# Kernel optimization log

Measured on AMD Instinct MI355X. Metric: run time of the kernel, lower is better.

## Reference

```python
import jax, jax.numpy as jnp
import numpy as np

LN_EPS = 1e-5

def layer_norm(h, gamma, beta):
    mu = jnp.mean(h, axis=-1, keepdims=True)
    var = jnp.mean(jnp.square(h - mu), axis=-1, keepdims=True)
    return (h - mu) * jax.lax.rsqrt(var + LN_EPS) * gamma + beta

def gcn_conv(x, src, dst, W, b, n_nodes):
    # PyG GCNConv: h = X W; out = D^-1/2 (A + I) D^-1/2 h + b
    h = x @ W
    deg = jax.ops.segment_sum(jnp.ones_like(src, dtype=h.dtype), dst, num_segments=n_nodes)
    dinv = jax.lax.rsqrt(jnp.maximum(deg, 1.0))  # deg >= 1 due to self-loops
    norm = dinv[src] * dinv[dst]                  # [E]
    msg = h[src] * norm[:, None]                  # [E, d]
    return jax.ops.segment_sum(msg, dst, num_segments=n_nodes) + b

def setup_inputs() -> dict:
    key = jax.random.key(0)
    ks = jax.random.split(key, 8)
    N, E, Cin, Ch, Cout = 10000, 160000, 256, 512, 256
    x = jax.random.normal(ks[0], (N, Cin), dtype=jnp.float32)
    edge_index = jax.random.randint(ks[1], (2, E), 0, N, dtype=jnp.int64)
    W1 = jax.random.normal(ks[2], (Cin, Ch), dtype=jnp.float32) * (1.0 / np.sqrt(Cin))
    b1 = jnp.zeros((Ch,), dtype=jnp.float32)
    gamma1 = jnp.ones((Ch,), dtype=jnp.float32)
    beta1 = jnp.zeros((Ch,), dtype=jnp.float32)
    W2 = jax.random.normal(ks[3], (Ch, Cout), dtype=jnp.float32) * (1.0 / np.sqrt(Ch))
    b2 = jnp.zeros((Cout,), dtype=jnp.float32)
    gamma2 = jnp.ones((Cout,), dtype=jnp.float32)
    beta2 = jnp.zeros((Cout,), dtype=jnp.float32)
    return {"x": x, "edge_index": edge_index, "W1": W1, "b1": b1,
            "gamma1": gamma1, "beta1": beta1, "W2": W2, "b2": b2,
            "gamma2": gamma2, "beta2": beta2}

def reference(x, edge_index, W1, b1, gamma1, beta1, W2, b2, gamma2, beta2):
    n = x.shape[0]
    loops = jnp.arange(n, dtype=edge_index.dtype)
    src = jnp.concatenate([edge_index[0], loops])
    dst = jnp.concatenate([edge_index[1], loops])
    h = gcn_conv(x, src, dst, W1, b1, n)
    h = jax.nn.relu(layer_norm(h, gamma1, beta1))  # dropout = identity (eval mode)
    g = gcn_conv(h, src, dst, W2, b2, n)
    g = jax.nn.relu(layer_norm(g, gamma2, beta2))
    return g
```

## Files before the change

### kernel.cpp

```cpp
#include <hip/hip_runtime.h>
#include <hip/hip_bf16.h>


typedef __attribute__((ext_vector_type(8))) short bf16x8;
typedef __attribute__((ext_vector_type(4))) float f32x4;
typedef __attribute__((ext_vector_type(4))) unsigned short us4;

__device__ __forceinline__ unsigned short f2bf(float f) {
  unsigned int x = __float_as_uint(f);
  return (unsigned short)((x + 0x7FFFu + ((x >> 16) & 1u)) >> 16);
}

__device__ __forceinline__ void wave_reduce2(float& s, float& ss) {
#pragma unroll
  for (int off = 32; off > 0; off >>= 1) {
    s  += __shfl_down(s, off, 64);
    ss += __shfl_down(ss, off, 64);
  }
}


__global__ __launch_bounds__(256) void deg_kernel(const int* __restrict__ dst, int E,
                                                  int* __restrict__ deg) {
  int e = blockIdx.x * 256 + threadIdx.x;
  if (e < E) atomicAdd(&deg[dst[e]], 1);
}

__global__ __launch_bounds__(256) void dinv_kernel(const int* __restrict__ deg, int N,
                                                   float* __restrict__ dinv) {
  int i = blockIdx.x * 256 + threadIdx.x;
  if (i < N) dinv[i] = rsqrtf((float)(deg[i] + 1));
}

__global__ __launch_bounds__(1024) void scan_kernel(const int* __restrict__ deg, int N,
                                                    int* __restrict__ offsets) {
  __shared__ int wsum[16];
  __shared__ int chunk_base;
  int tid = threadIdx.x;
  int lane = tid & 63, wid = tid >> 6;
  if (tid == 0) chunk_base = 0;
  __syncthreads();
  for (int c = 0; c < N; c += 1024) {
    int i = c + tid;
    int v = (i < N) ? deg[i] : 0;
    int s = v;
#pragma unroll
    for (int off = 1; off < 64; off <<= 1) {
      int t = __shfl_up(s, off, 64);
      if (lane >= off) s += t;
    }
    if (lane == 63) wsum[wid] = s;
    __syncthreads();
    if (wid == 0 && lane < 16) {
      int ws = wsum[lane];
      int t = ws;
#pragma unroll
      for (int off = 1; off < 16; off <<= 1) {
        int u = __shfl_up(t, off, 64);
        if (lane >= off) t += u;
      }
      wsum[lane] = t - ws;
    }
    __syncthreads();
    if (i < N) offsets[i] = chunk_base + wsum[wid] + s - v;
    __syncthreads();
    if (tid == 1023) chunk_base += wsum[15] + s;
  }
  __syncthreads();
  if (tid == 0) offsets[N] = chunk_base;
}

__global__ __launch_bounds__(256) void fill_kernel(const int* __restrict__ src,
                                                   const int* __restrict__ dst, int E,
                                                   const int* __restrict__ offsets,
                                                   int* __restrict__ cursor,
                                                   const float* __restrict__ dinv,
                                                   int* __restrict__ csr_src,
                                                   float* __restrict__ csr_norm) {
  int e = blockIdx.x * 256 + threadIdx.x;
  if (e >= E) return;
  int s = src[e], d = dst[e];
  int p = offsets[d] + atomicAdd(&cursor[d], 1);
  csr_src[p]  = s;
  csr_norm[p] = dinv[s] * dinv[d];
}


template <typename OutT>
__global__ __launch_bounds__(256) void agg_kernel(const float* __restrict__ H,
                                                  const int* __restrict__ csr_src,
                                                  const float* __restrict__ csr_norm,
                                                  const int* __restrict__ offsets,
                                                  const float* __restrict__ dinv,
                                                  const float* __restrict__ bias,
                                                  OutT* __restrict__ out) {
  __shared__ f32x4 sh[256];
  int node = blockIdx.x;
  int tid = threadIdx.x, w = tid >> 6, c4 = tid & 63;
  int p0 = offsets[node], p1 = offsets[node + 1];
  f32x4 acc = {0.f, 0.f, 0.f, 0.f};
  for (int p = p0 + w; p < p1; p += 4) {
    int s   = csr_src[p];
    float wt = csr_norm[p];
    f32x4 h = *(const f32x4*)&H[(size_t)s * 256 + c4 * 4];
    acc += h * wt;
  }
  sh[tid] = acc;
  __syncthreads();
  if (tid < 64) {
    f32x4 a = sh[tid] + sh[64 + tid] + sh[128 + tid] + sh[192 + tid];
    float dn = dinv[node];
    f32x4 self = *(const f32x4*)&H[(size_t)node * 256 + tid * 4];
    a += self * (dn * dn);
    if (bias) a += *(const f32x4*)&bias[tid * 4];
    if constexpr (sizeof(OutT) == 4) {
      *(f32x4*)&out[(size_t)node * 256 + tid * 4] = a;
    } else {
      us4 o;
      o.x = f2bf(a.x); o.y = f2bf(a.y); o.z = f2bf(a.z); o.w = f2bf(a.w);
      *(us4*)&out[(size_t)node * 256 + tid * 4] = o;
    }
  }
}

__global__ __launch_bounds__(256) void transpose_bf16(const float* __restrict__ W,
                                                      unsigned short* __restrict__ Wt,
                                                      int K, int N) {
  __shared__ unsigned short t[32][33];
  int n0 = blockIdx.x * 32, k0 = blockIdx.y * 32;
  int tx = threadIdx.x & 31, ty = threadIdx.x >> 5;
#pragma unroll
  for (int i = 0; i < 32; i += 8)
    t[ty + i][tx] = f2bf(W[(size_t)(k0 + ty + i) * N + n0 + tx]);
  __syncthreads();
#pragma unroll
  for (int i = 0; i < 32; i += 8)
    Wt[(size_t)(n0 + ty + i) * K + k0 + tx] = t[tx][ty + i];
}


__global__ __launch_bounds__(256) void mfma_gemm_kernel(
    const unsigned short* __restrict__ A, const unsigned short* __restrict__ Bt,
    const float* __restrict__ bias, float* __restrict__ C, int M, int K, int N) {
  __shared__ unsigned short As[128 * 32];
  __shared__ unsigned short Bs[128 * 32];
  int tid = threadIdx.x;
  int lane = tid & 63, wid = tid >> 6;
  int bm = blockIdx.x * 128, bn = blockIdx.y * 128;
  int wm = (wid >> 1) * 64, wn = (wid & 1) * 64;
  int srow = tid >> 2;
  int schunk = tid & 3;
  int frow = lane & 15, fk = lane >> 4;
  f32x4 acc[4][4] = {};

  for (int k0 = 0; k0 < K; k0 += 32) {
#pragma unroll
    for (int r = 0; r < 2; ++r) {
      int row = r * 64 + srow;
      int scA = schunk ^ ((row >> 1) & 3);
      int ga = bm + row; ga = ga < M ? ga : M - 1;
      int gb = bn + row; gb = gb < N ? gb : N - 1;
      const unsigned short* gA = A + (size_t)ga * K + k0 + scA * 8;
      const unsigned short* gB = Bt + (size_t)gb * K + k0 + scA * 8;
      __builtin_amdgcn_global_load_lds(
          (const __attribute__((address_space(1))) unsigned int*)(const void*)gA,
          (__attribute__((address_space(3))) unsigned int*)(void*)(As + (r * 64 + wid * 16) * 32),
          16, 0, 0);
      __builtin_amdgcn_global_load_lds(
          (const __attribute__((address_space(1))) unsigned int*)(const void*)gB,
          (__attribute__((address_space(3))) unsigned int*)(void*)(Bs + (r * 64 + wid * 16) * 32),
          16, 0, 0);
    }
    __syncthreads();
    bf16x8 af[4], bf[4];
#pragma unroll
    for (int mi = 0; mi < 4; ++mi) {
      int row = wm + mi * 16 + frow;
      int sc = fk ^ ((row >> 1) & 3);
      af[mi] = *(const bf16x8*)(As + row * 32 + sc * 8);
    }
#pragma unroll
    for (int ni = 0; ni < 4; ++ni) {
      int row = wn + ni * 16 + frow;
      int sc = fk ^ ((row >> 1) & 3);
      bf[ni] = *(const bf16x8*)(Bs + row * 32 + sc * 8);
    }
#pragma unroll
    for (int mi = 0; mi < 4; ++mi)
#pragma unroll
      for (int ni = 0; ni < 4; ++ni)
        acc[mi][ni] = __builtin_amdgcn_mfma_f32_16x16x32_bf16(af[mi], bf[ni], acc[mi][ni], 0, 0, 0);
    __syncthreads();
  }

  int row0 = bm + wm + (lane >> 4) * 4;
  int col0 = bn + wn + (lane & 15);
#pragma unroll
  for (int mi = 0; mi < 4; ++mi) {
#pragma unroll
    for (int ni = 0; ni < 4; ++ni) {
      int col = col0 + ni * 16;
      float bv = bias ? bias[col] : 0.0f;
#pragma unroll
      for (int r = 0; r < 4; ++r) {
        int row = row0 + mi * 16 + r;
        if (row < M) C[(size_t)row * N + col] = acc[mi][ni][r] + bv;
      }
    }
  }
}


template <int C, typename OutT>
__global__ __launch_bounds__(256) void ln_relu_kernel(const float* __restrict__ in,
                                                      const float* __restrict__ gamma,
                                                      const float* __restrict__ beta,
                                                      OutT* __restrict__ out) {
  int row = blockIdx.x;
  const float* p = in + (size_t)row * C;
  int tid = threadIdx.x;
  float v0 = p[tid];
  float v1 = (C == 512) ? p[tid + 256] : 0.0f;
  float s = v0 + v1;
  float ss = v0 * v0 + v1 * v1;
  wave_reduce2(s, ss);
  __shared__ float sh[8];
  int wid = tid >> 6;
  if ((tid & 63) == 0) { sh[wid] = s; sh[4 + wid] = ss; }
  __syncthreads();
  s  = sh[0] + sh[1] + sh[2] + sh[3];
  ss = sh[4] + sh[5] + sh[6] + sh[7];
  float mu = s * (1.0f / C);
  float var = ss * (1.0f / C) - mu * mu;
  float r = rsqrtf(var + 1e-5f);
  float o0 = fmaxf((v0 - mu) * r * gamma[tid] + beta[tid], 0.0f);
  if constexpr (sizeof(OutT) == 4) out[(size_t)row * C + tid] = o0;
  else                             out[(size_t)row * C + tid] = f2bf(o0);
  if (C == 512) {
    float o1 = fmaxf((v1 - mu) * r * gamma[tid + 256] + beta[tid + 256], 0.0f);
    if constexpr (sizeof(OutT) == 4) out[(size_t)row * C + tid + 256] = o1;
    else                             out[(size_t)row * C + tid + 256] = f2bf(o1);
  }
}


extern "C" void kernel_launch(void* const* d_in, const int* in_sizes, int n_in,
                              void* d_out, int out_size, void* d_ws, size_t ws_size,
                              hipStream_t stream) {
  const float* x    = (const float*)d_in[0];
  const int*   ei   = (const int*)d_in[1];
  const float* W1   = (const float*)d_in[2];
  const float* b1   = (const float*)d_in[3];
  const float* ga1  = (const float*)d_in[4];
  const float* be1  = (const float*)d_in[5];
  const float* W2   = (const float*)d_in[6];
  const float* b2   = (const float*)d_in[7];
  const float* ga2  = (const float*)d_in[8];
  const float* be2  = (const float*)d_in[9];
  float* out = (float*)d_out;

  const int Ch   = in_sizes[3];
  const int Cout = in_sizes[7];
  const int Cin  = in_sizes[2] / Ch;
  const int N    = in_sizes[0] / Cin;
  const int E    = in_sizes[1] / 2;
  const int* srcp = ei;
  const int* dstp = ei + E;

  char* ws = (char*)d_ws;
  size_t off = 0;
  auto alloc = [&](size_t bytes) -> void* {
    off = (off + 255) & ~(size_t)255;
    void* p = ws + off;
    off += bytes;
    return p;
  };
  unsigned short* axb  = (unsigned short*)alloc((size_t)N * Cin * 2);
  float*          h1   = (float*)alloc((size_t)N * Ch * 4);
  unsigned short* h1b  = (unsigned short*)alloc((size_t)N * Ch * 2);
  float*          h2   = (float*)alloc((size_t)N * Cout * 4);
  unsigned short* W1t  = (unsigned short*)alloc((size_t)Cin * Ch * 2);
  unsigned short* W2t  = (unsigned short*)alloc((size_t)Ch * Cout * 2);
  int*   deg   = (int*)alloc((size_t)N * 4);
  int*   curs  = (int*)alloc((size_t)N * 4);
  int*   offs  = (int*)alloc((size_t)(N + 1) * 4);
  float* dinv  = (float*)alloc((size_t)N * 4);
  int*   csr_s = (int*)alloc((size_t)E * 4);
  float* csr_n = (float*)alloc((size_t)E * 4);

  hipMemsetAsync(deg, 0, (size_t)N * 4, stream);
  hipMemsetAsync(curs, 0, (size_t)N * 4, stream);

  int gE = (E + 255) / 256;
  int gN = (N + 255) / 256;
  deg_kernel<<<gE, 256, 0, stream>>>(dstp, E, deg);
  dinv_kernel<<<gN, 256, 0, stream>>>(deg, N, dinv);
  scan_kernel<<<1, 1024, 0, stream>>>(deg, N, offs);
  fill_kernel<<<gE, 256, 0, stream>>>(srcp, dstp, E, offs, curs, dinv, csr_s, csr_n);

  transpose_bf16<<<dim3(Ch / 32, Cin / 32), 256, 0, stream>>>(W1, W1t, Cin, Ch);
  transpose_bf16<<<dim3(Cout / 32, Ch / 32), 256, 0, stream>>>(W2, W2t, Ch, Cout);

  agg_kernel<unsigned short><<<N, 256, 0, stream>>>(x, csr_s, csr_n, offs, dinv, nullptr, axb);
  mfma_gemm_kernel<<<dim3((N + 127) / 128, Ch / 128), 256, 0, stream>>>(axb, W1t, b1, h1, N, Cin, Ch);
  ln_relu_kernel<512, unsigned short><<<N, 256, 0, stream>>>(h1, ga1, be1, h1b);

  mfma_gemm_kernel<<<dim3((N + 127) / 128, Cout / 128), 256, 0, stream>>>(h1b, W2t, nullptr, h2, N, Ch, Cout);
  agg_kernel<float><<<N, 256, 0, stream>>>(h2, csr_s, csr_n, offs, dinv, b2, h1);
  ln_relu_kernel<256, float><<<N, 256, 0, stream>>>(h1, ga2, be2, out);
}
```

Before: 222.0 us.

## Fuse preprocessing kernels, gather bf16 features, fuse final LayerNorm into aggregation

Merges the degree count, the x-to-bf16 cast and both weight transposes into one multi-role prep kernel, and folds dinv computation and cursor initialisation into the scan. Aggregation now gathers bf16 rows instead of fp32, which halves gather traffic. The second GEMM writes bf16 output, and the final LayerNorm+ReLU is fused into the second aggregation kernel. This removes several launches and intermediate round trips through memory, at the cost of extra bf16 rounding on the gathered features and one more workspace buffer.

Measured after the change: 208.4 us. 1.07x faster.

```diff
diff --git a/kernel.cpp b/kernel.cpp
--- a/kernel.cpp
+++ b/kernel.cpp
@@ -5,35 +5,68 @@
 typedef __attribute__((ext_vector_type(8))) short bf16x8;
 typedef __attribute__((ext_vector_type(4))) float f32x4;
 typedef __attribute__((ext_vector_type(4))) unsigned short us4;
+typedef __attribute__((ext_vector_type(8))) unsigned short us8;
 
 __device__ __forceinline__ unsigned short f2bf(float f) {
   unsigned int x = __float_as_uint(f);
   return (unsigned short)((x + 0x7FFFu + ((x >> 16) & 1u)) >> 16);
 }
-
-__device__ __forceinline__ void wave_reduce2(float& s, float& ss) {
-#pragma unroll
-  for (int off = 32; off > 0; off >>= 1) {
-    s  += __shfl_down(s, off, 64);
-    ss += __shfl_down(ss, off, 64);
-  }
-}
-
-
-__global__ __launch_bounds__(256) void deg_kernel(const int* __restrict__ dst, int E,
-                                                  int* __restrict__ deg) {
-  int e = blockIdx.x * 256 + threadIdx.x;
-  if (e < E) atomicAdd(&deg[dst[e]], 1);
-}
-
-__global__ __launch_bounds__(256) void dinv_kernel(const int* __restrict__ deg, int N,
-                                                   float* __restrict__ dinv) {
-  int i = blockIdx.x * 256 + threadIdx.x;
-  if (i < N) dinv[i] = rsqrtf((float)(deg[i] + 1));
+__device__ __forceinline__ float bf2f(unsigned short u) {
+  return __uint_as_float((unsigned int)u << 16);
+}
+
+
+__device__ __forceinline__ void transpose_tile(const float* __restrict__ W,
+                                               unsigned short* __restrict__ Wt,
+                                               int K, int N, int n0, int k0,
+                                               unsigned short (*t)[33], int tid) {
+  int tx = tid & 31, ty = tid >> 5;
+#pragma unroll
+  for (int i = 0; i < 32; i += 8)
+    t[ty + i][tx] = f2bf(W[(size_t)(k0 + ty + i) * N + n0 + tx]);
+  __syncthreads();
+#pragma unroll
+  for (int i = 0; i < 32; i += 8)
+    Wt[(size_t)(n0 + ty + i) * K + k0 + tx] = t[tx][ty + i];
+}
+
+__global__ __launch_bounds__(256) void prep_kernel(
+    const float* __restrict__ x, unsigned short* __restrict__ xb, long nelem,
+    const int* __restrict__ dst, int E, int* __restrict__ deg,
+    const float* __restrict__ W1, unsigned short* __restrict__ W1t,
+    const float* __restrict__ W2, unsigned short* __restrict__ W2t,
+    int Cin, int Ch, int Cout, int nbx, int nbe, int nbw1) {
+  __shared__ unsigned short t[32][33];
+  int bid = blockIdx.x;
+  int tid = threadIdx.x;
+  if (bid < nbx) {
+    long i = ((long)bid * 256 + tid) * 8;
+    if (i + 8 <= nelem) {
+      f32x4 a = *(const f32x4*)&x[i];
+      f32x4 b = *(const f32x4*)&x[i + 4];
+      us8 o;
+      o[0] = f2bf(a.x); o[1] = f2bf(a.y); o[2] = f2bf(a.z); o[3] = f2bf(a.w);
+      o[4] = f2bf(b.x); o[5] = f2bf(b.y); o[6] = f2bf(b.z); o[7] = f2bf(b.w);
+      *(us8*)&xb[i] = o;
+    }
+  } else if (bid < nbx + nbe) {
+    int e = (bid - nbx) * 256 + tid;
+    if (e < E) atomicAdd(&deg[dst[e]], 1);
+  } else if (bid < nbx + nbe + nbw1) {
+    int ti = bid - nbx - nbe;
+    int w1w = Ch >> 5;
+    transpose_tile(W1, W1t, Cin, Ch, (ti % w1w) * 32, (ti / w1w) * 32, t, tid);
+  } else {
+    int ti = bid - nbx - nbe - nbw1;
+    int w2w = Cout >> 5;
+    transpose_tile(W2, W2t, Ch, Cout, (ti % w2w) * 32, (ti / w2w) * 32, t, tid);
+  }
 }
 
 __global__ __launch_bounds__(1024) void scan_kernel(const int* __restrict__ deg, int N,
-                                                    int* __restrict__ offsets) {
+                                                    int* __restrict__ offsets,
+                                                    int* __restrict__ curs,
+                                                    float* __restrict__ dinv) {
   __shared__ int wsum[16];
   __shared__ int chunk_base;
   int tid = threadIdx.x;
@@ -43,6 +76,7 @@
   for (int c = 0; c < N; c += 1024) {
     int i = c + tid;
     int v = (i < N) ? deg[i] : 0;
+    if (i < N) dinv[i] = rsqrtf((float)(v + 1));
     int s = v;
 #pragma unroll
     for (int off = 1; off < 64; off <<= 1) {
@@ -62,7 +96,11 @@
       wsum[lane] = t - ws;
     }
     __syncthreads();
-    if (i < N) offsets[i] = chunk_base + wsum[wid] + s - v;
+    if (i < N) {
+      int o = chunk_base + wsum[wid] + s - v;
+      offsets[i] = o;
+      curs[i] = o;
+    }
     __syncthreads();
     if (tid == 1023) chunk_base += wsum[15] + s;
   }
@@ -72,27 +110,28 @@
 
 __global__ __launch_bounds__(256) void fill_kernel(const int* __restrict__ src,
                                                    const int* __restrict__ dst, int E,
-                                                   const int* __restrict__ offsets,
-                                                   int* __restrict__ cursor,
+                                                   int* __restrict__ curs,
                                                    const float* __restrict__ dinv,
                                                    int* __restrict__ csr_src,
                                                    float* __restrict__ csr_norm) {
   int e = blockIdx.x * 256 + threadIdx.x;
   if (e >= E) return;
   int s = src[e], d = dst[e];
-  int p = offsets[d] + atomicAdd(&cursor[d], 1);
+  int p = atomicAdd(&curs[d], 1);
   csr_src[p]  = s;
   csr_norm[p] = dinv[s] * dinv[d];
 }
 
 
-template <typename OutT>
-__global__ __launch_bounds__(256) void agg_kernel(const float* __restrict__ H,
+template <bool FUSE_LN, typename OutT>
+__global__ __launch_bounds__(256) void agg_kernel(const unsigned short* __restrict__ H,
                                                   const int* __restrict__ csr_src,
                                                   const float* __restrict__ csr_norm,
                                                   const int* __restrict__ offsets,
                                                   const float* __restrict__ dinv,
                                                   const float* __restrict__ bias,
+                                                  const float* __restrict__ gamma,
+                                                  const float* __restrict__ beta,
                                                   OutT* __restrict__ out) {
   __shared__ f32x4 sh[256];
   int node = blockIdx.x;
@@ -100,21 +139,45 @@
   int p0 = offsets[node], p1 = offsets[node + 1];
   f32x4 acc = {0.f, 0.f, 0.f, 0.f};
   for (int p = p0 + w; p < p1; p += 4) {
-    int s   = csr_src[p];
+    int s    = csr_src[p];
     float wt = csr_norm[p];
-    f32x4 h = *(const f32x4*)&H[(size_t)s * 256 + c4 * 4];
-    acc += h * wt;
+    us4 hv = *(const us4*)&H[(size_t)s * 256 + c4 * 4];
+    acc.x = fmaf(bf2f(hv.x), wt, acc.x);
+    acc.y = fmaf(bf2f(hv.y), wt, acc.y);
+    acc.z = fmaf(bf2f(hv.z), wt, acc.z);
+    acc.w = fmaf(bf2f(hv.w), wt, acc.w);
   }
   sh[tid] = acc;
   __syncthreads();
   if (tid < 64) {
     f32x4 a = sh[tid] + sh[64 + tid] + sh[128 + tid] + sh[192 + tid];
     float dn = dinv[node];
-    f32x4 self = *(const f32x4*)&H[(size_t)node * 256 + tid * 4];
-    a += self * (dn * dn);
+    float w2 = dn * dn;
+    us4 sv = *(const us4*)&H[(size_t)node * 256 + tid * 4];
+    a.x = fmaf(bf2f(sv.x), w2, a.x);
+    a.y = fmaf(bf2f(sv.y), w2, a.y);
+    a.z = fmaf(bf2f(sv.z), w2, a.z);
+    a.w = fmaf(bf2f(sv.w), w2, a.w);
     if (bias) a += *(const f32x4*)&bias[tid * 4];
-    if constexpr (sizeof(OutT) == 4) {
-      *(f32x4*)&out[(size_t)node * 256 + tid * 4] = a;
+    if constexpr (FUSE_LN) {
+      float s  = a.x + a.y + a.z + a.w;
+      float ss = a.x * a.x + a.y * a.y + a.z * a.z + a.w * a.w;
+#pragma unroll
+      for (int off = 32; off > 0; off >>= 1) {
+        s  += __shfl_xor(s, off, 64);
+        ss += __shfl_xor(ss, off, 64);
+      }
+      float mu = s * (1.0f / 256.0f);
+      float var = ss * (1.0f / 256.0f) - mu * mu;
+      float r = rsqrtf(var + 1e-5f);
+      f32x4 g  = *(const f32x4*)&gamma[tid * 4];
+      f32x4 be = *(const f32x4*)&beta[tid * 4];
+      f32x4 o;
+      o.x = fmaxf((a.x - mu) * r * g.x + be.x, 0.f);
+      o.y = fmaxf((a.y - mu) * r * g.y + be.y, 0.f);
+      o.z = fmaxf((a.z - mu) * r * g.z + be.z, 0.f);
+      o.w = fmaxf((a.w - mu) * r * g.w + be.w, 0.f);
+      *(f32x4*)&out[(size_t)node * 256 + tid * 4] = o;
     } else {
       us4 o;
       o.x = f2bf(a.x); o.y = f2bf(a.y); o.z = f2bf(a.z); o.w = f2bf(a.w);
@@ -123,25 +186,11 @@
   }
 }
 
-__global__ __launch_bounds__(256) void transpose_bf16(const float* __restrict__ W,
-                                                      unsigned short* __restrict__ Wt,
-                                                      int K, int N) {
-  __shared__ unsigned short t[32][33];
-  int n0 = blockIdx.x * 32, k0 = blockIdx.y * 32;
-  int tx = threadIdx.x & 31, ty = threadIdx.x >> 5;
-#pragma unroll
-  for (int i = 0; i < 32; i += 8)
-    t[ty + i][tx] = f2bf(W[(size_t)(k0 + ty + i) * N + n0 + tx]);
-  __syncthreads();
-#pragma unroll
-  for (int i = 0; i < 32; i += 8)
-    Wt[(size_t)(n0 + ty + i) * K + k0 + tx] = t[tx][ty + i];
-}
-
-
+
+template <typename OutT>
 __global__ __launch_bounds__(256) void mfma_gemm_kernel(
     const unsigned short* __restrict__ A, const unsigned short* __restrict__ Bt,
-    const float* __restrict__ bias, float* __restrict__ C, int M, int K, int N) {
+    const float* __restrict__ bias, OutT* __restrict__ C, int M, int K, int N) {
   __shared__ unsigned short As[128 * 32];
   __shared__ unsigned short Bs[128 * 32];
   int tid = threadIdx.x;
@@ -204,43 +253,44 @@
 #pragma unroll
       for (int r = 0; r < 4; ++r) {
         int row = row0 + mi * 16 + r;
-        if (row < M) C[(size_t)row * N + col] = acc[mi][ni][r] + bv;
+        if (row < M) {
+          float v = acc[mi][ni][r] + bv;
+          if constexpr (sizeof(OutT) == 4) C[(size_t)row * N + col] = v;
+          else                             C[(size_t)row * N + col] = f2bf(v);
+        }
       }
     }
   }
 }
 
 
-template <int C, typename OutT>
-__global__ __launch_bounds__(256) void ln_relu_kernel(const float* __restrict__ in,
-                                                      const float* __restrict__ gamma,
-                                                      const float* __restrict__ beta,
-                                                      OutT* __restrict__ out) {
+__global__ __launch_bounds__(256) void ln_relu512_kernel(const float* __restrict__ in,
+                                                         const float* __restrict__ gamma,
+                                                         const float* __restrict__ beta,
+                                                         unsigned short* __restrict__ out) {
   int row = blockIdx.x;
-  const float* p = in + (size_t)row * C;
+  const float* p = in + (size_t)row * 512;
   int tid = threadIdx.x;
   float v0 = p[tid];
-  float v1 = (C == 512) ? p[tid + 256] : 0.0f;
+  float v1 = p[tid + 256];
   float s = v0 + v1;
   float ss = v0 * v0 + v1 * v1;
-  wave_reduce2(s, ss);
+#pragma unroll
+  for (int off = 32; off > 0; off >>= 1) {
+    s  += __shfl_down(s, off, 64);
+    ss += __shfl_down(ss, off, 64);
+  }
   __shared__ float sh[8];
   int wid = tid >> 6;
   if ((tid & 63) == 0) { sh[wid] = s; sh[4 + wid] = ss; }
   __syncthreads();
   s  = sh[0] + sh[1] + sh[2] + sh[3];
   ss = sh[4] + sh[5] + sh[6] + sh[7];
-  float mu = s * (1.0f / C);
-  float var = ss * (1.0f / C) - mu * mu;
+  float mu = s * (1.0f / 512.0f);
+  float var = ss * (1.0f / 512.0f) - mu * mu;
   float r = rsqrtf(var + 1e-5f);
-  float o0 = fmaxf((v0 - mu) * r * gamma[tid] + beta[tid], 0.0f);
-  if constexpr (sizeof(OutT) == 4) out[(size_t)row * C + tid] = o0;
-  else                             out[(size_t)row * C + tid] = f2bf(o0);
-  if (C == 512) {
-    float o1 = fmaxf((v1 - mu) * r * gamma[tid + 256] + beta[tid + 256], 0.0f);
-    if constexpr (sizeof(OutT) == 4) out[(size_t)row * C + tid + 256] = o1;
-    else                             out[(size_t)row * C + tid + 256] = f2bf(o1);
-  }
+  out[(size_t)row * 512 + tid]       = f2bf(fmaxf((v0 - mu) * r * gamma[tid] + beta[tid], 0.0f));
+  out[(size_t)row * 512 + tid + 256] = f2bf(fmaxf((v1 - mu) * r * gamma[tid + 256] + beta[tid + 256], 0.0f));
 }
 
 
@@ -275,10 +325,11 @@
     off += bytes;
     return p;
   };
+  unsigned short* xb   = (unsigned short*)alloc((size_t)N * Cin * 2);
   unsigned short* axb  = (unsigned short*)alloc((size_t)N * Cin * 2);
   float*          h1   = (float*)alloc((size_t)N * Ch * 4);
   unsigned short* h1b  = (unsigned short*)alloc((size_t)N * Ch * 2);
-  float*          h2   = (float*)alloc((size_t)N * Cout * 4);
+  unsigned short* h2b  = (unsigned short*)alloc((size_t)N * Cout * 2);
   unsigned short* W1t  = (unsigned short*)alloc((size_t)Cin * Ch * 2);
   unsigned short* W2t  = (unsigned short*)alloc((size_t)Ch * Cout * 2);
   int*   deg   = (int*)alloc((size_t)N * 4);
@@ -289,23 +340,25 @@
   float* csr_n = (float*)alloc((size_t)E * 4);
 
   hipMemsetAsync(deg, 0, (size_t)N * 4, stream);
-  hipMemsetAsync(curs, 0, (size_t)N * 4, stream);
-
-  int gE = (E + 255) / 256;
-  int gN = (N + 255) / 256;
-  deg_kernel<<<gE, 256, 0, stream>>>(dstp, E, deg);
-  dinv_kernel<<<gN, 256, 0, stream>>>(deg, N, dinv);
-  scan_kernel<<<1, 1024, 0, stream>>>(deg, N, offs);
-  fill_kernel<<<gE, 256, 0, stream>>>(srcp, dstp, E, offs, curs, dinv, csr_s, csr_n);
-
-  transpose_bf16<<<dim3(Ch / 32, Cin / 32), 256, 0, stream>>>(W1, W1t, Cin, Ch);
-  transpose_bf16<<<dim3(Cout / 32, Ch / 32), 256, 0, stream>>>(W2, W2t, Ch, Cout);
-
-  agg_kernel<unsigned short><<<N, 256, 0, stream>>>(x, csr_s, csr_n, offs, dinv, nullptr, axb);
-  mfma_gemm_kernel<<<dim3((N + 127) / 128, Ch / 128), 256, 0, stream>>>(axb, W1t, b1, h1, N, Cin, Ch);
-  ln_relu_kernel<512, unsigned short><<<N, 256, 0, stream>>>(h1, ga1, be1, h1b);
-
-  mfma_gemm_kernel<<<dim3((N + 127) / 128, Cout / 128), 256, 0, stream>>>(h1b, W2t, nullptr, h2, N, Ch, Cout);
-  agg_kernel<float><<<N, 256, 0, stream>>>(h2, csr_s, csr_n, offs, dinv, b2, h1);
-  ln_relu_kernel<256, float><<<N, 256, 0, stream>>>(h1, ga2, be2, out);
-}
+
+  long nelem = (long)N * Cin;
+  int nbx  = (int)((nelem / 8 + 255) / 256);
+  int nbe  = (E + 255) / 256;
+  int nbw1 = (Cin / 32) * (Ch / 32);
+  int nbw2 = (Ch / 32) * (Cout / 32);
+  prep_kernel<<<nbx + nbe + nbw1 + nbw2, 256, 0, stream>>>(
+      x, xb, nelem, dstp, E, deg, W1, W1t, W2, W2t, Cin, Ch, Cout, nbx, nbe, nbw1);
+  scan_kernel<<<1, 1024, 0, stream>>>(deg, N, offs, curs, dinv);
+  fill_kernel<<<nbe, 256, 0, stream>>>(srcp, dstp, E, curs, dinv, csr_s, csr_n);
+
+  agg_kernel<false, unsigned short><<<N, 256, 0, stream>>>(
+      xb, csr_s, csr_n, offs, dinv, nullptr, nullptr, nullptr, axb);
+  mfma_gemm_kernel<float><<<dim3((N + 127) / 128, Ch / 128), 256, 0, stream>>>(
+      axb, W1t, b1, h1, N, Cin, Ch);
+  ln_relu512_kernel<<<N, 256, 0, stream>>>(h1, ga1, be1, h1b);
+
+  mfma_gemm_kernel<unsigned short><<<dim3((N + 127) / 128, Cout / 128), 256, 0, stream>>>(
+      h1b, W2t, nullptr, h2b, N, Ch, Cout);
+  agg_kernel<true, float><<<N, 256, 0, stream>>>(
+      h2b, csr_s, csr_n, offs, dinv, b2, ga2, be2, out);
+}
```
